# Optimization experiments

Measured on AMD Instinct MI355X. Metric: run time of the kernel, lower is better.

## Reference

```python
import jax, jax.numpy as jnp
import numpy as np

NUM_HEADS = 8
NUM_GROUPS = 8
NUM_ITERATIONS = 3
DT = 0.1
EPS = 1e-5


def group_norm(x, scale, bias):
    # x: [B, C, H, W], GroupNorm(8, C)
    B, C, H, W = x.shape
    xg = x.reshape(B, NUM_GROUPS, C // NUM_GROUPS, H, W)
    mean = xg.mean(axis=(2, 3, 4), keepdims=True)
    var = xg.var(axis=(2, 3, 4), keepdims=True)
    xg = (xg - mean) * jax.lax.rsqrt(var + EPS)
    x = xg.reshape(B, C, H, W)
    return x * scale[None, :, None, None] + bias[None, :, None, None]


def setup_inputs() -> dict:
    key = jax.random.key(0)
    ks = jax.random.split(key, 4)
    B, C, H, W = 8, 512, 32, 32
    x = jax.random.normal(ks[0], (B, C, H, W), dtype=jnp.float32)
    qkv_w = jax.random.normal(ks[1], (3 * C, C), dtype=jnp.float32) * (1.0 / np.sqrt(C))
    proj_w = jax.random.normal(ks[2], (C, C), dtype=jnp.float32) * (1.0 / np.sqrt(C))
    inl_w = jax.random.normal(ks[3], (C, C), dtype=jnp.float32) * (1.0 / np.sqrt(C))
    return {
        "x": x,
        "gn_scale": jnp.ones((C,), jnp.float32),
        "gn_bias": jnp.zeros((C,), jnp.float32),
        "qkv_w": qkv_w,
        "qkv_b": jnp.zeros((3 * C,), jnp.float32),
        "proj_w": proj_w,
        "proj_b": jnp.zeros((C,), jnp.float32),
        "inl_w": inl_w,
        "inl_b": jnp.zeros((C,), jnp.float32),
    }


def reference(x, gn_scale, gn_bias, qkv_w, qkv_b, proj_w, proj_b, inl_w, inl_b):
    B, C, H, W = x.shape
    nh = NUM_HEADS
    hd = C // nh
    S = H * W

    h = group_norm(x, gn_scale, gn_bias)

    # 1x1 conv == channel matmul
    qkv = jnp.einsum('oc,bchw->bohw', qkv_w, h) + qkv_b[None, :, None, None]
    q, k, v = jnp.split(qkv, 3, axis=1)  # each [B, C, H, W]

    def to_heads(t):  # [B, C, H, W] -> [B, nh, S, hd]
        return t.reshape(B, nh, hd, S).transpose(0, 1, 3, 2)

    q, k, v = to_heads(q), to_heads(k), to_heads(v)

    scale = hd ** (-0.5)
    attn = jax.nn.softmax(jnp.einsum('bnsd,bntd->bnst', q, k) * scale, axis=-1)
    h = jnp.einsum('bnst,bntd->bnsd', attn, v)  # [B, nh, S, hd]

    # back to [B, S, C] for INL refinement
    h_flat = h.transpose(0, 1, 3, 2).reshape(B, C, S).transpose(0, 2, 1)

    # SimpleINLDynamics: iterative Euler refinement x <- x + dt * tanh(W x + b)
    def step(hf, _):
        hf = hf + DT * jnp.tanh(jnp.einsum('bsc,oc->bso', hf, inl_w) + inl_b)
        return hf, None
    h_flat, _ = jax.lax.scan(step, h_flat, None, length=NUM_ITERATIONS)

    h = h_flat.transpose(0, 2, 1).reshape(B, C, H, W)
    h = jnp.einsum('oc,bchw->bohw', proj_w, h) + proj_b[None, :, None, None]
    return x + h
```

## Files before the change

### kernel.cpp

```cpp
#include <hip/hip_runtime.h>
#include <math.h>

#define B_ 8
#define C_ 512
#define S_ 1024
#define HD 64
#define NHEADS 8
#define NGROUPS 8
#define DT_STEP 0.1f
#define EPS_GN 1e-5f
#define LOG2E 1.4426950408889634f

typedef __attribute__((ext_vector_type(8))) short bf16x8;
typedef __attribute__((ext_vector_type(4))) float f32x4;
typedef __attribute__((ext_vector_type(8))) unsigned short ushort8;
typedef __attribute__((ext_vector_type(4))) unsigned short ushort4_t;

static __device__ __forceinline__ unsigned short f2bf(float f) {
  unsigned int u = __builtin_bit_cast(unsigned int, f);
  u += 0x7fff + ((u >> 16) & 1);
  return (unsigned short)(u >> 16);
}

static __device__ __forceinline__ unsigned short f2bf_fast(float f) {
  unsigned int u = __builtin_bit_cast(unsigned int, f);
  return (unsigned short)((u + 0x8000u) >> 16);
}

static __device__ __forceinline__ float bf2f(unsigned short u) {
  unsigned int t = ((unsigned int)u) << 16;
  return __builtin_bit_cast(float, t);
}

static __device__ __forceinline__ float exp2_raw(float x) {
  return __builtin_amdgcn_exp2f(x);
}

static __device__ __forceinline__ float fast_tanh(float x) {
  float xc = fminf(fmaxf(x, -15.f), 15.f);
  float e = exp2_raw(xc * (2.0f * LOG2E));
  return (e - 1.f) / (e + 1.f);
}

__global__ __launch_bounds__(256) void prep_kernel(
    const float* __restrict__ a, const float* __restrict__ b, const float* __restrict__ c,
    unsigned short* __restrict__ A, unsigned short* __restrict__ B, unsigned short* __restrict__ C,
    const float* __restrict__ x, float* __restrict__ gpart) {
  int bid = blockIdx.x;
  int tid = threadIdx.x;
  if (bid < 640) {
    const float* src; unsigned short* dst; int off;
    if (bid < 384) { src = a; dst = A; off = bid * 2048; }
    else if (bid < 512) { src = b; dst = B; off = (bid - 384) * 2048; }
    else { src = c; dst = C; off = (bid - 512) * 2048; }
    int i = off + tid * 8;
    f32x4 v0 = *(const f32x4*)(src + i);
    f32x4 v1 = *(const f32x4*)(src + i + 4);
    ushort8 o;
    o[0] = f2bf(v0[0]); o[1] = f2bf(v0[1]); o[2] = f2bf(v0[2]); o[3] = f2bf(v0[3]);
    o[4] = f2bf(v1[0]); o[5] = f2bf(v1[1]); o[6] = f2bf(v1[2]); o[7] = f2bf(v1[3]);
    *(ushort8*)(dst + i) = o;
    return;
  }
  int sbid = bid - 640;
  int bg = sbid >> 3, chunk = sbid & 7;
  const float* xp = x + (size_t)bg * 65536 + (size_t)chunk * 8192;
  float sum = 0.f, sq = 0.f;
  #pragma unroll
  for (int i = 0; i < 8; ++i) {
    f32x4 v = *(const f32x4*)(xp + i * 1024 + tid * 4);
    sum += v[0] + v[1] + v[2] + v[3];
    sq += v[0]*v[0] + v[1]*v[1] + v[2]*v[2] + v[3]*v[3];
  }
  #pragma unroll
  for (int off = 32; off >= 1; off >>= 1) {
    sum += __shfl_xor(sum, off, 64);
    sq  += __shfl_xor(sq, off, 64);
  }
  __shared__ float s1[4], s2[4];
  int wave = tid >> 6, lane = tid & 63;
  if (lane == 0) { s1[wave] = sum; s2[wave] = sq; }
  __syncthreads();
  if (tid == 0) {
    float S = s1[0] + s1[1] + s1[2] + s1[3];
    float Q = s2[0] + s2[1] + s2[2] + s2[3];
    gpart[bg * 16 + chunk * 2] = S;
    gpart[bg * 16 + chunk * 2 + 1] = Q;
  }
}

__global__ __launch_bounds__(256) void gn_apply_t(
    const float* __restrict__ x, const float* __restrict__ gpart,
    const float* __restrict__ scale, const float* __restrict__ bias,
    unsigned short* __restrict__ h_t) {
  int bid = blockIdx.x;
  int bg = bid >> 4, st = bid & 15;
  int b = bg >> 3, g = bg & 7;
  float S = 0.f, Q = 0.f;
  #pragma unroll
  for (int i = 0; i < 8; ++i) {
    S += gpart[bg * 16 + i * 2];
    Q += gpart[bg * 16 + i * 2 + 1];
  }
  float mean = S / 65536.f;
  float var = Q / 65536.f - mean * mean;
  float inv = rsqrtf(var + EPS_GN);

  int tid = threadIdx.x;
  int sl = tid >> 2;
  int cq = (tid & 3) * 16;
  float sA[16], sB[16];
  #pragma unroll
  for (int u = 0; u < 16; ++u) {
    float scv = scale[g * 64 + cq + u];
    sA[u] = inv * scv;
    sB[u] = bias[g * 64 + cq + u] - mean * inv * scv;
  }

  const float* xp = x + ((size_t)b * C_ + (size_t)g * 64) * S_;
  __shared__ float tile[64][65];
  #pragma unroll
  for (int it = 0; it < 16; ++it) {
    int lin = it * 256 + tid;
    int c = lin >> 6, s = lin & 63;
    tile[c][s] = xp[(size_t)c * S_ + st * 64 + s];
  }
  __syncthreads();
  unsigned short vals[16];
  #pragma unroll
  for (int u = 0; u < 16; ++u)
    vals[u] = f2bf_fast(tile[cq + u][sl] * sA[u] + sB[u]);
  unsigned short* dst = h_t + ((size_t)b * S_ + st * 64 + sl) * C_ + g * 64 + cq;
  ushort8 lo, hi;
  #pragma unroll
  for (int u = 0; u < 8; ++u) { lo[u] = vals[u]; hi[u] = vals[u + 8]; }
  *(ushort8*)dst = lo;
  *(ushort8*)(dst + 8) = hi;
}

template<int MB, int NB, int WMG, int WNG>
__device__ __forceinline__ void gemm_nt_core(
    const unsigned short* __restrict__ Ab,
    const unsigned short* __restrict__ Bb,
    unsigned short* ldsA, unsigned short* ldsB,
    f32x4* acc) {
  constexpr int TI = (MB / WMG) / 16;
  constexpr int TJ = (NB / WNG) / 16;
  constexpr int NQA = MB * 4 / 256;
  constexpr int NQB = NB * 4 / 256;
  const int K = 512;
  const int tid = threadIdx.x;
  const int w = tid >> 6, lane = tid & 63, quad = lane >> 4, l15 = lane & 15;
  const int wm = (WNG == 1) ? w : ((WMG == 1) ? 0 : (w >> 1));
  const int wn = (WNG == 1) ? 0 : ((WMG == 1) ? w : (w & 1));

  ushort8 apf[NQA], bpf[NQB];
  #pragma unroll
  for (int q = 0; q < NQA; ++q) {
    int c = q * 256 + tid;
    apf[q] = *(const ushort8*)(Ab + (size_t)(c >> 2) * K + (c & 3) * 8);
  }
  #pragma unroll
  for (int q = 0; q < NQB; ++q) {
    int c = q * 256 + tid;
    bpf[q] = *(const ushort8*)(Bb + (size_t)(c >> 2) * K + (c & 3) * 8);
  }

  for (int k0 = 0; k0 < K; k0 += 32) {
    __syncthreads();
    #pragma unroll
    for (int q = 0; q < NQA; ++q) {
      int c = q * 256 + tid;
      *(ushort8*)(ldsA + c * 8) = apf[q];
    }
    #pragma unroll
    for (int q = 0; q < NQB; ++q) {
      int c = q * 256 + tid;
      *(ushort8*)(ldsB + c * 8) = bpf[q];
    }
    __syncthreads();
    if (k0 + 32 < K) {
      #pragma unroll
      for (int q = 0; q < NQA; ++q) {
        int c = q * 256 + tid;
        apf[q] = *(const ushort8*)(Ab + (size_t)(c >> 2) * K + k0 + 32 + (c & 3) * 8);
      }
      #pragma unroll
      for (int q = 0; q < NQB; ++q) {
        int c = q * 256 + tid;
        bpf[q] = *(const ushort8*)(Bb + (size_t)(c >> 2) * K + k0 + 32 + (c & 3) * 8);
      }
    }
    bf16x8 af[TI], bfr[TJ];
    #pragma unroll
    for (int i = 0; i < TI; ++i)
      af[i] = *(const bf16x8*)(ldsA + (wm * (MB / WMG) + i * 16 + l15) * 32 + quad * 8);
    #pragma unroll
    for (int j = 0; j < TJ; ++j)
      bfr[j] = *(const bf16x8*)(ldsB + (wn * (NB / WNG) + j * 16 + l15) * 32 + quad * 8);
    #pragma unroll
    for (int i = 0; i < TI; ++i)
      #pragma unroll
      for (int j = 0; j < TJ; ++j)
        acc[i * TJ + j] = __builtin_amdgcn_mfma_f32_16x16x32_bf16(af[i], bfr[j], acc[i * TJ + j], 0, 0, 0);
  }
}

__global__ __launch_bounds__(256) void gemm_qkv_mfma(
    const unsigned short* __restrict__ Wbf, const unsigned short* __restrict__ h_t,
    const float* __restrict__ bias,
    unsigned short* __restrict__ Qt, unsigned short* __restrict__ Kt,
    unsigned short* __restrict__ Vt) {
  __shared__ __align__(16) unsigned short ldsA[128 * 32];
  __shared__ __align__(16) unsigned short ldsB[128 * 32];
  int b = blockIdx.z;
  int bm = blockIdx.y * 128, bn = blockIdx.x * 128;
  f32x4 acc[16];
  #pragma unroll
  for (int t = 0; t < 16; ++t) acc[t] = (f32x4){0.f, 0.f, 0.f, 0.f};
  gemm_nt_core<128, 128, 2, 2>(Wbf + (size_t)bm * 512,
                               h_t + ((size_t)b * S_ + bn) * 512, ldsA, ldsB, acc);
  int tid = threadIdx.x, w = tid >> 6, lane = tid & 63, quad = lane >> 4, l15 = lane & 15;
  int wm = w >> 1, wn = w & 1;
  int tensor = bm >> 9;
  float qscale = (tensor == 0) ? 0.125f * LOG2E : 1.0f;
  #pragma unroll
  for (int i = 0; i < 4; ++i) {
    #pragma unroll
    for (int j = 0; j < 4; ++j) {
      int m0 = bm + wm * 64 + i * 16 + quad * 4;
      int ng = bn + wn * 64 + j * 16 + l15;
      f32x4 v = acc[i * 4 + j];
      if (tensor < 2) {
        int head = (m0 >> 6) & 7, d0 = m0 & 63;
        ushort4_t pk;
        #pragma unroll
        for (int r = 0; r < 4; ++r) pk[r] = f2bf((v[r] + bias[m0 + r]) * qscale);
        unsigned short* dst = (tensor ? Kt : Qt) +
            (((size_t)(b * 8 + head) * S_ + ng) * 64 + d0);
        *(ushort4_t*)dst = pk;
      } else {
        #pragma unroll
        for (int r = 0; r < 4; ++r)
          Vt[(size_t)b * (C_ * S_) + (size_t)(m0 - 1024 + r) * S_ + ng] = f2bf(v[r] + bias[m0 + r]);
      }
    }
  }
}

__global__ __launch_bounds__(256) void attn_mfma(
    const unsigned short* __restrict__ Qt,
    const unsigned short* __restrict__ Kt,
    const unsigned short* __restrict__ Vt,
    unsigned short* __restrict__ hflat_bf) {
  int tid = threadIdx.x, wave = tid >> 6, lane = tid & 63;
  int quad = lane >> 4, l15 = lane & 15;
  int bid = blockIdx.x;
  int bn = bid & 63, sblk = bid >> 6, b = bn >> 3, n = bn & 7;
  int s0w = sblk * 128 + wave * 32;

  __shared__ unsigned short k_lds[64][72];
  __shared__ unsigned short v_lds[64][72];
  __shared__ unsigned short p_lds[4][2][16][72];

  const unsigned short* Kb = Kt + ((size_t)(b * 8 + n)) * S_ * 64;
  const unsigned short* Vb = Vt + ((size_t)b * C_ + n * 64) * S_;

  bf16x8 qa[2][2];
  #pragma unroll
  for (int g = 0; g < 2; ++g) {
    const unsigned short* Qb = Qt + (((size_t)(b * 8 + n)) * S_ + s0w + g * 16 + l15) * 64;
    qa[g][0] = *(const bf16x8*)(Qb + quad * 8);
    qa[g][1] = *(const bf16x8*)(Qb + 32 + quad * 8);
  }

  bf16x8 ones;
  #pragma unroll
  for (int j = 0; j < 8; ++j) ones[j] = (short)0x3F80;

  f32x4 o_acc[2][4];
  f32x4 l_acc[2];
  #pragma unroll
  for (int g = 0; g < 2; ++g) {
    l_acc[g] = (f32x4){0.f, 0.f, 0.f, 0.f};
    #pragma unroll
    for (int dc = 0; dc < 4; ++dc) o_acc[g][dc] = (f32x4){0.f, 0.f, 0.f, 0.f};
  }

  int row0 = tid >> 3, c80 = (tid & 7) * 8;
  int row1 = (tid + 256) >> 3, c81 = c80;

  ushort8 kreg[2], vreg[2];
  kreg[0] = *(const ushort8*)(Kb + (size_t)row0 * 64 + c80);
  kreg[1] = *(const ushort8*)(Kb + (size_t)row1 * 64 + c81);
  vreg[0] = *(const ushort8*)(Vb + (size_t)row0 * S_ + c80);
  vreg[1] = *(const ushort8*)(Vb + (size_t)row1 * S_ + c81);

  for (int t0 = 0; t0 < S_; t0 += 64) {
    __syncthreads();
    *(ushort8*)&k_lds[row0][c80] = kreg[0];
    *(ushort8*)&k_lds[row1][c81] = kreg[1];
    *(ushort8*)&v_lds[row0][c80] = vreg[0];
    *(ushort8*)&v_lds[row1][c81] = vreg[1];
    __syncthreads();
    if (t0 + 64 < S_) {
      int t1 = t0 + 64;
      kreg[0] = *(const ushort8*)(Kb + (size_t)(t1 + row0) * 64 + c80);
      kreg[1] = *(const ushort8*)(Kb + (size_t)(t1 + row1) * 64 + c81);
      vreg[0] = *(const ushort8*)(Vb + (size_t)row0 * S_ + t1 + c80);
      vreg[1] = *(const ushort8*)(Vb + (size_t)row1 * S_ + t1 + c81);
    }

    f32x4 sc[2][4];
    #pragma unroll
    for (int tc = 0; tc < 4; ++tc) {
      bf16x8 kb0 = *(const bf16x8*)&k_lds[tc * 16 + l15][quad * 8];
      bf16x8 kb1 = *(const bf16x8*)&k_lds[tc * 16 + l15][32 + quad * 8];
      #pragma unroll
      for (int g = 0; g < 2; ++g) {
        f32x4 c = {0.f, 0.f, 0.f, 0.f};
        c = __builtin_amdgcn_mfma_f32_16x16x32_bf16(kb0, qa[g][0], c, 0, 0, 0);
        sc[g][tc] = __builtin_amdgcn_mfma_f32_16x16x32_bf16(kb1, qa[g][1], c, 0, 0, 0);
      }
    }

    #pragma unroll
    for (int g = 0; g < 2; ++g)
      #pragma unroll
      for (int tc = 0; tc < 4; ++tc) {
        ushort4_t p4;
        #pragma unroll
        for (int r = 0; r < 4; ++r) p4[r] = f2bf_fast(exp2_raw(sc[g][tc][r]));
        *(ushort4_t*)&p_lds[wave][g][l15][tc * 16 + quad * 4] = p4;
      }

    bf16x8 pa[2][2];
    #pragma unroll
    for (int g = 0; g < 2; ++g) {
      pa[g][0] = *(const bf16x8*)&p_lds[wave][g][l15][quad * 8];
      pa[g][1] = *(const bf16x8*)&p_lds[wave][g][l15][32 + quad * 8];
      l_acc[g] = __builtin_amdgcn_mfma_f32_16x16x32_bf16(pa[g][0], ones, l_acc[g], 0, 0, 0);
      l_acc[g] = __builtin_amdgcn_mfma_f32_16x16x32_bf16(pa[g][1], ones, l_acc[g], 0, 0, 0);
    }
    #pragma unroll
    for (int dc = 0; dc < 4; ++dc) {
      bf16x8 vb0 = *(const bf16x8*)&v_lds[dc * 16 + l15][quad * 8];
      bf16x8 vb1 = *(const bf16x8*)&v_lds[dc * 16 + l15][32 + quad * 8];
      #pragma unroll
      for (int g = 0; g < 2; ++g) {
        o_acc[g][dc] = __builtin_amdgcn_mfma_f32_16x16x32_bf16(pa[g][0], vb0, o_acc[g][dc], 0, 0, 0);
        o_acc[g][dc] = __builtin_amdgcn_mfma_f32_16x16x32_bf16(pa[g][1], vb1, o_acc[g][dc], 0, 0, 0);
      }
    }
  }

  #pragma unroll
  for (int g = 0; g < 2; ++g) {
    float inv_l[4];
    #pragma unroll
    for (int r = 0; r < 4; ++r) inv_l[r] = 1.f / l_acc[g][r];
    #pragma unroll
    for (int dc = 0; dc < 4; ++dc) {
      #pragma unroll
      for (int r = 0; r < 4; ++r) {
        int s = s0w + g * 16 + quad * 4 + r;
        size_t idx = ((size_t)b * S_ + s) * C_ + n * 64 + dc * 16 + l15;
        hflat_bf[idx] = f2bf_fast(o_acc[g][dc][r] * inv_l[r]);
      }
    }
  }
}

__global__ __launch_bounds__(256) void inl_step_mfma(
    const unsigned short* __restrict__ hbf_in, const unsigned short* __restrict__ Wbf,
    const float* __restrict__ bias, unsigned short* __restrict__ hbf_out) {
  __shared__ __align__(16) unsigned short ldsA[64 * 32];
  __shared__ __align__(16) unsigned short ldsB[64 * 32];
  int bm = blockIdx.y * 64, bn = blockIdx.x * 64;
  f32x4 acc[4];
  #pragma unroll
  for (int t = 0; t < 4; ++t) acc[t] = (f32x4){0.f, 0.f, 0.f, 0.f};
  gemm_nt_core<64, 64, 2, 2>(hbf_in + (size_t)bm * 512,
                             Wbf + (size_t)bn * 512, ldsA, ldsB, acc);
  int tid = threadIdx.x, w = tid >> 6, lane = tid & 63, quad = lane >> 4, l15 = lane & 15;
  int wm = w >> 1, wn = w & 1;
  #pragma unroll
  for (int i = 0; i < 2; ++i) {
    #pragma unroll
    for (int j = 0; j < 2; ++j) {
      int m0 = bm + wm * 32 + i * 16 + quad * 4;
      int o = bn + wn * 32 + j * 16 + l15;
      float bv = bias[o];
      f32x4 v = acc[i * 2 + j];
      #pragma unroll
      for (int r = 0; r < 4; ++r) {
        size_t idx = (size_t)(m0 + r) * 512 + o;
        float hin = bf2f(hbf_in[idx]);
        hbf_out[idx] = f2bf_fast(hin + DT_STEP * fast_tanh(v[r] + bv));
      }
    }
  }
}

__global__ __launch_bounds__(256) void gemm_proj_mfma(
    const unsigned short* __restrict__ Wbf, const unsigned short* __restrict__ hbf,
    const float* __restrict__ pb, const float* __restrict__ x,
    float* __restrict__ Out) {
  __shared__ __align__(16) unsigned short ldsA[64 * 32];
  __shared__ __align__(16) unsigned short ldsB[64 * 32];
  int bm = blockIdx.y * 64, bn = blockIdx.x * 64;
  f32x4 acc[4];
  #pragma unroll
  for (int t = 0; t < 4; ++t) acc[t] = (f32x4){0.f, 0.f, 0.f, 0.f};
  gemm_nt_core<64, 64, 2, 2>(Wbf + (size_t)bm * 512,
                             hbf + (size_t)bn * 512, ldsA, ldsB, acc);
  int tid = threadIdx.x, w = tid >> 6, lane = tid & 63, quad = lane >> 4, l15 = lane & 15;
  int wm = w >> 1, wn = w & 1;
  #pragma unroll
  for (int i = 0; i < 2; ++i) {
    #pragma unroll
    for (int j = 0; j < 2; ++j) {
      int o0 = bm + wm * 32 + i * 16 + quad * 4;
      int ng = bn + wn * 32 + j * 16 + l15;
      int b = ng >> 10, s = ng & 1023;
      f32x4 v = acc[i * 2 + j];
      #pragma unroll
      for (int r = 0; r < 4; ++r) {
        size_t idx = ((size_t)b * C_ + o0 + r) * S_ + s;
        Out[idx] = x[idx] + pb[o0 + r] + v[r];
      }
    }
  }
}

extern "C" void kernel_launch(void* const* d_in, const int* in_sizes, int n_in,
                              void* d_out, int out_size, void* d_ws, size_t ws_size,
                              hipStream_t stream) {
  const float* x        = (const float*)d_in[0];
  const float* gn_scale = (const float*)d_in[1];
  const float* gn_bias  = (const float*)d_in[2];
  const float* qkv_w    = (const float*)d_in[3];
  const float* qkv_b    = (const float*)d_in[4];
  const float* proj_w   = (const float*)d_in[5];
  const float* proj_b   = (const float*)d_in[6];
  const float* inl_w    = (const float*)d_in[7];
  const float* inl_b    = (const float*)d_in[8];
  float* out = (float*)d_out;
  float* ws = (float*)d_ws;

  unsigned short* Qt  = (unsigned short*)(ws + 8388608);
  unsigned short* Kt  = (unsigned short*)(ws + 10485760);
  unsigned short* Vt  = (unsigned short*)(ws + 12582912);
  unsigned short* h_t = (unsigned short*)(ws + 14680064);
  unsigned short* Bbf = h_t;
  unsigned short* Abf = (unsigned short*)(ws + 16777216);
  float* gpart = ws + 18874368;
  unsigned short* qkvw_bf  = (unsigned short*)(ws + 18878464);
  unsigned short* inlw_bf  = qkvw_bf + 786432;
  unsigned short* projw_bf = inlw_bf + 262144;

  prep_kernel<<<1152, 256, 0, stream>>>(qkv_w, inl_w, proj_w, qkvw_bf, inlw_bf, projw_bf, x, gpart);
  gn_apply_t<<<1024, 256, 0, stream>>>(x, gpart, gn_scale, gn_bias, h_t);
  gemm_qkv_mfma<<<dim3(8, 12, 8), 256, 0, stream>>>(qkvw_bf, h_t, qkv_b, Qt, Kt, Vt);
  attn_mfma<<<512, 256, 0, stream>>>(Qt, Kt, Vt, Abf);
  inl_step_mfma<<<dim3(8, 128), 256, 0, stream>>>(Abf, inlw_bf, inl_b, Bbf);
  inl_step_mfma<<<dim3(8, 128), 256, 0, stream>>>(Bbf, inlw_bf, inl_b, Abf);
  inl_step_mfma<<<dim3(8, 128), 256, 0, stream>>>(Abf, inlw_bf, inl_b, Bbf);
  gemm_proj_mfma<<<dim3(128, 8), 256, 0, stream>>>(projw_bf, Bbf, proj_b, x, out);
}
```

Measured before the change: 205.4 us.

## Fuse three INL Euler steps and output projection into one row-resident kernel

Replaces three separate INL step GEMM launches and the projection GEMM with a single kernel. Each block keeps a 32-row slab of the hidden state in LDS across all four matmuls and streams weights directly from global memory. The INL and projection weights are pre-swizzled into 32-column slabs so each lane can load contiguous bf16x8 fragments. This removes three intermediate global round-trips of the activations and three launches. In exchange it uses only 256 blocks with uncached weight reads per block, which may limit occupancy and raise L2 traffic.

```diff
diff --git a/kernel.cpp b/kernel.cpp
--- a/kernel.cpp
+++ b/kernel.cpp
@@ -48,10 +48,20 @@
     const float* __restrict__ x, float* __restrict__ gpart) {
   int bid = blockIdx.x;
   int tid = threadIdx.x;
+  if (bid < 384) {
+    int off = bid * 2048;
+    int i = off + tid * 8;
+    f32x4 v0 = *(const f32x4*)(a + i);
+    f32x4 v1 = *(const f32x4*)(a + i + 4);
+    ushort8 o;
+    o[0] = f2bf(v0[0]); o[1] = f2bf(v0[1]); o[2] = f2bf(v0[2]); o[3] = f2bf(v0[3]);
+    o[4] = f2bf(v1[0]); o[5] = f2bf(v1[1]); o[6] = f2bf(v1[2]); o[7] = f2bf(v1[3]);
+    *(ushort8*)(A + i) = o;
+    return;
+  }
   if (bid < 640) {
     const float* src; unsigned short* dst; int off;
-    if (bid < 384) { src = a; dst = A; off = bid * 2048; }
-    else if (bid < 512) { src = b; dst = B; off = (bid - 384) * 2048; }
+    if (bid < 512) { src = b; dst = B; off = (bid - 384) * 2048; }
     else { src = c; dst = C; off = (bid - 512) * 2048; }
     int i = off + tid * 8;
     f32x4 v0 = *(const f32x4*)(src + i);
@@ -59,7 +69,9 @@
     ushort8 o;
     o[0] = f2bf(v0[0]); o[1] = f2bf(v0[1]); o[2] = f2bf(v0[2]); o[3] = f2bf(v0[3]);
     o[4] = f2bf(v1[0]); o[5] = f2bf(v1[1]); o[6] = f2bf(v1[2]); o[7] = f2bf(v1[3]);
-    *(ushort8*)(dst + i) = o;
+    int orow = i >> 9, cbase = i & 511;
+    int dsti = (cbase >> 5) * 16384 + orow * 32 + (cbase & 31);
+    *(ushort8*)(dst + dsti) = o;
     return;
   }
   int sbid = bid - 640;
@@ -371,66 +383,92 @@
   }
 }
 
-__global__ __launch_bounds__(256) void inl_step_mfma(
-    const unsigned short* __restrict__ hbf_in, const unsigned short* __restrict__ Wbf,
-    const float* __restrict__ bias, unsigned short* __restrict__ hbf_out) {
-  __shared__ __align__(16) unsigned short ldsA[64 * 32];
-  __shared__ __align__(16) unsigned short ldsB[64 * 32];
-  int bm = blockIdx.y * 64, bn = blockIdx.x * 64;
-  f32x4 acc[4];
-  #pragma unroll
-  for (int t = 0; t < 4; ++t) acc[t] = (f32x4){0.f, 0.f, 0.f, 0.f};
-  gemm_nt_core<64, 64, 2, 2>(hbf_in + (size_t)bm * 512,
-                             Wbf + (size_t)bn * 512, ldsA, ldsB, acc);
-  int tid = threadIdx.x, w = tid >> 6, lane = tid & 63, quad = lane >> 4, l15 = lane & 15;
-  int wm = w >> 1, wn = w & 1;
-  #pragma unroll
-  for (int i = 0; i < 2; ++i) {
-    #pragma unroll
-    for (int j = 0; j < 2; ++j) {
-      int m0 = bm + wm * 32 + i * 16 + quad * 4;
-      int o = bn + wn * 32 + j * 16 + l15;
-      float bv = bias[o];
-      f32x4 v = acc[i * 2 + j];
-      #pragma unroll
-      for (int r = 0; r < 4; ++r) {
-        size_t idx = (size_t)(m0 + r) * 512 + o;
-        float hin = bf2f(hbf_in[idx]);
-        hbf_out[idx] = f2bf_fast(hin + DT_STEP * fast_tanh(v[r] + bv));
-      }
-    }
-  }
-}
-
-__global__ __launch_bounds__(256) void gemm_proj_mfma(
-    const unsigned short* __restrict__ Wbf, const unsigned short* __restrict__ hbf,
-    const float* __restrict__ pb, const float* __restrict__ x,
-    float* __restrict__ Out) {
-  __shared__ __align__(16) unsigned short ldsA[64 * 32];
-  __shared__ __align__(16) unsigned short ldsB[64 * 32];
-  int bm = blockIdx.y * 64, bn = blockIdx.x * 64;
-  f32x4 acc[4];
-  #pragma unroll
-  for (int t = 0; t < 4; ++t) acc[t] = (f32x4){0.f, 0.f, 0.f, 0.f};
-  gemm_nt_core<64, 64, 2, 2>(Wbf + (size_t)bm * 512,
-                             hbf + (size_t)bn * 512, ldsA, ldsB, acc);
-  int tid = threadIdx.x, w = tid >> 6, lane = tid & 63, quad = lane >> 4, l15 = lane & 15;
-  int wm = w >> 1, wn = w & 1;
-  #pragma unroll
-  for (int i = 0; i < 2; ++i) {
-    #pragma unroll
-    for (int j = 0; j < 2; ++j) {
-      int o0 = bm + wm * 32 + i * 16 + quad * 4;
-      int ng = bn + wn * 32 + j * 16 + l15;
-      int b = ng >> 10, s = ng & 1023;
-      f32x4 v = acc[i * 2 + j];
-      #pragma unroll
-      for (int r = 0; r < 4; ++r) {
-        size_t idx = ((size_t)b * C_ + o0 + r) * S_ + s;
-        Out[idx] = x[idx] + pb[o0 + r] + v[r];
-      }
-    }
-  }
+__global__ __launch_bounds__(512) void inl_proj_chain(
+    const unsigned short* __restrict__ hbf,
+    const unsigned short* __restrict__ Wi2,
+    const unsigned short* __restrict__ Wp2,
+    const float* __restrict__ ib, const float* __restrict__ pb,
+    const float* __restrict__ x, float* __restrict__ Out) {
+  __shared__ __align__(16) unsigned short h_lds[32][520];
+
+  int tid = threadIdx.x;
+  int wave = tid >> 6, lane = tid & 63, quad = lane >> 4, l15 = lane & 15;
+  int wo = wave * 64;
+  int bid = blockIdx.x;
+  int b = bid >> 5, s0 = (bid & 31) * 32;
+
+  const unsigned short* hsrc = hbf + (size_t)bid * 16384;
+  #pragma unroll
+  for (int it = 0; it < 4; ++it) {
+    int lin = it * 512 + tid;
+    ushort8 v = *(const ushort8*)(hsrc + (size_t)lin * 8);
+    *(ushort8*)&h_lds[lin >> 6][(lin & 63) * 8] = v;
+  }
+
+  float bias_i[4], bias_p[4];
+  #pragma unroll
+  for (int j = 0; j < 4; ++j) {
+    bias_i[j] = ib[wo + j * 16 + l15];
+    bias_p[j] = pb[wo + j * 16 + l15];
+  }
+
+  f32x4 acc[2][4];
+  #pragma unroll
+  for (int i = 0; i < 2; ++i)
+    #pragma unroll
+    for (int j = 0; j < 4; ++j) acc[i][j] = (f32x4){0.f, 0.f, 0.f, 0.f};
+
+  __syncthreads();
+
+  for (int step = 0; step < 4; ++step) {
+    const unsigned short* Wb = (step < 3) ? Wi2 : Wp2;
+    #pragma unroll 4
+    for (int slab = 0; slab < 16; ++slab) {
+      const unsigned short* wp = Wb + slab * 16384;
+      bf16x8 afr[2], bfr[4];
+      #pragma unroll
+      for (int i = 0; i < 2; ++i)
+        afr[i] = *(const bf16x8*)&h_lds[i * 16 + l15][slab * 32 + quad * 8];
+      #pragma unroll
+      for (int j = 0; j < 4; ++j)
+        bfr[j] = *(const bf16x8*)(wp + (size_t)(wo + j * 16 + l15) * 32 + quad * 8);
+      #pragma unroll
+      for (int i = 0; i < 2; ++i)
+        #pragma unroll
+        for (int j = 0; j < 4; ++j)
+          acc[i][j] = __builtin_amdgcn_mfma_f32_16x16x32_bf16(afr[i], bfr[j], acc[i][j], 0, 0, 0);
+    }
+    if (step < 3) {
+      __syncthreads();
+      #pragma unroll
+      for (int i = 0; i < 2; ++i)
+        #pragma unroll
+        for (int j = 0; j < 4; ++j) {
+          int o = wo + j * 16 + l15;
+          #pragma unroll
+          for (int r = 0; r < 4; ++r) {
+            int s = i * 16 + quad * 4 + r;
+            float hv = bf2f(h_lds[s][o]);
+            h_lds[s][o] = f2bf_fast(hv + DT_STEP * fast_tanh(acc[i][j][r] + bias_i[j]));
+            acc[i][j][r] = 0.f;
+          }
+        }
+      __syncthreads();
+    }
+  }
+
+  #pragma unroll
+  for (int i = 0; i < 2; ++i)
+    #pragma unroll
+    for (int j = 0; j < 4; ++j) {
+      int o = wo + j * 16 + l15;
+      size_t base = (((size_t)b * 512 + o) << 10) + (size_t)(s0 + i * 16 + quad * 4);
+      f32x4 xv = *(const f32x4*)(x + base);
+      f32x4 ov;
+      #pragma unroll
+      for (int r = 0; r < 4; ++r) ov[r] = xv[r] + bias_p[j] + acc[i][j][r];
+      *(f32x4*)(Out + base) = ov;
+    }
 }
 
 extern "C" void kernel_launch(void* const* d_in, const int* in_sizes, int n_in,
@@ -452,7 +490,6 @@
   unsigned short* Kt  = (unsigned short*)(ws + 10485760);
   unsigned short* Vt  = (unsigned short*)(ws + 12582912);
   unsigned short* h_t = (unsigned short*)(ws + 14680064);
-  unsigned short* Bbf = h_t;
   unsigned short* Abf = (unsigned short*)(ws + 16777216);
   float* gpart = ws + 18874368;
   unsigned short* qkvw_bf  = (unsigned short*)(ws + 18878464);
@@ -463,8 +500,5 @@
   gn_apply_t<<<1024, 256, 0, stream>>>(x, gpart, gn_scale, gn_bias, h_t);
   gemm_qkv_mfma<<<dim3(8, 12, 8), 256, 0, stream>>>(qkvw_bf, h_t, qkv_b, Qt, Kt, Vt);
   attn_mfma<<<512, 256, 0, stream>>>(Qt, Kt, Vt, Abf);
-  inl_step_mfma<<<dim3(8, 128), 256, 0, stream>>>(Abf, inlw_bf, inl_b, Bbf);
-  inl_step_mfma<<<dim3(8, 128), 256, 0, stream>>>(Bbf, inlw_bf, inl_b, Abf);
-  inl_step_mfma<<<dim3(8, 128), 256, 0, stream>>>(Abf, inlw_bf, inl_b, Bbf);
-  gemm_proj_mfma<<<dim3(128, 8), 256, 0, stream>>>(projw_bf, Bbf, proj_b, x, out);
-}
+  inl_proj_chain<<<256, 512, 0, stream>>>(Abf, inlw_bf, projw_bf, inl_b, proj_b, x, out);
+}
```

Result: faster. 193.4 us (-5.8%).
